# Kernel tuning notes

Measured on AMD Instinct MI355X. Metric: run time of the kernel, lower is better.

The kernel has to match this reference:

```python
import jax, jax.numpy as jnp
import numpy as np

NEG_SLOPE = 0.01
NUM_GRAPHS = 4096


def _gcn(x, W, b, src, dst, ew, n_nodes):
    # GCNConv(normalize=False): linear transform, then weighted scatter-add to targets, plus bias
    h = x @ W                                  # [N, out]
    msg = h[src] * ew[:, None]                 # [E, out] gather + scale
    agg = jax.ops.segment_sum(msg, dst, num_segments=n_nodes)  # scatter-add
    return agg + b


def setup_inputs() -> dict:
    key = jax.random.key(0)
    ks = jax.random.split(key, 24)
    N, E = 253952, 4000000
    x = jax.random.normal(ks[0], (N, 6), dtype=jnp.float32)
    edge_index = jax.random.randint(ks[1], (2, E), 0, N, dtype=jnp.int64)
    edge_weight = jax.random.uniform(ks[2], (E,), dtype=jnp.float32)
    batch = jnp.sort(jax.random.randint(ks[3], (N,), 0, NUM_GRAPHS, dtype=jnp.int64))

    def lin(k, fi, fo):
        k1, k2 = jax.random.split(k)
        s = 1.0 / np.sqrt(fi)
        return (jax.random.normal(k1, (fi, fo), dtype=jnp.float32) * s,
                jax.random.normal(k2, (fo,), dtype=jnp.float32) * s)

    W1, b1 = lin(ks[4], 6, 16)
    W2, b2 = lin(ks[5], 16, 32)
    W3, b3 = lin(ks[6], 32, 64)
    W4, b4 = lin(ks[7], 64, 50)
    Wf1, bf1 = lin(ks[8], 50, 30)
    Wf2, bf2 = lin(ks[9], 30, 20)
    Wf3, bf3 = lin(ks[10], 20, 2)
    return {"x": x, "edge_index": edge_index, "edge_weight": edge_weight, "batch": batch,
            "W1": W1, "b1": b1, "W2": W2, "b2": b2, "W3": W3, "b3": b3, "W4": W4, "b4": b4,
            "Wf1": Wf1, "bf1": bf1, "Wf2": Wf2, "bf2": bf2, "Wf3": Wf3, "bf3": bf3}


def reference(x, edge_index, edge_weight, batch,
              W1, b1, W2, b2, W3, b3, W4, b4,
              Wf1, bf1, Wf2, bf2, Wf3, bf3):
    lrelu = lambda v: jax.nn.leaky_relu(v, NEG_SLOPE)
    src, dst = edge_index[0], edge_index[1]
    n = x.shape[0]
    h = lrelu(_gcn(x, W1, b1, src, dst, edge_weight, n))
    h = lrelu(_gcn(h, W2, b2, src, dst, edge_weight, n))
    h = lrelu(_gcn(h, W3, b3, src, dst, edge_weight, n))
    conv_out = lrelu(_gcn(h, W4, b4, src, dst, edge_weight, n))
    # original applies leaky_relu again (batch_norm is defined but never used)
    h = lrelu(conv_out)
    pooled = jax.ops.segment_sum(h, batch, num_segments=NUM_GRAPHS)  # global_add_pool -> [G, 50]
    out = lrelu(pooled @ Wf1 + bf1)
    # dropout p=0.2 skipped (eval mode)
    out = lrelu(out @ Wf2 + bf2)
    out = lrelu(out @ Wf3 + bf3)
    return out
```

## Files before the change

### kernel.cpp

```cpp
#include <hip/hip_runtime.h>

#define N_NODES 253952
#define N_EDGES 4000000
#define N_GRAPHS 4096
#define NEG_SLOPE 0.01f

#define NB   248
#define CAP  20480
#define EPB  4096
#define WSCALE (1.0f / 16383.0f)

__device__ __forceinline__ float lrelu(float v) {
    return v > 0.0f ? v : v * NEG_SLOPE;
}

__device__ __forceinline__ unsigned short f2bf(float f) {
    unsigned b = __float_as_uint(f);
    return (unsigned short)((b + 0x7FFF + ((b >> 16) & 1)) >> 16);
}

__device__ __forceinline__ float bf2f(unsigned short h) {
    return __uint_as_float((unsigned)h << 16);
}

__device__ __forceinline__ void fma_bf16x8(float acc[8], const uint4 v, const float w) {
    acc[0] += __uint_as_float(v.x << 16) * w;
    acc[1] += __uint_as_float(v.x & 0xFFFF0000u) * w;
    acc[2] += __uint_as_float(v.y << 16) * w;
    acc[3] += __uint_as_float(v.y & 0xFFFF0000u) * w;
    acc[4] += __uint_as_float(v.z << 16) * w;
    acc[5] += __uint_as_float(v.z & 0xFFFF0000u) * w;
    acc[6] += __uint_as_float(v.w << 16) * w;
    acc[7] += __uint_as_float(v.w & 0xFFFF0000u) * w;
}

__global__ void pad_x_kernel(const float* __restrict__ x, unsigned short* __restrict__ xb,
                             int* __restrict__ bucket_cnt) {
    if (blockIdx.x == 0 && threadIdx.x < NB) bucket_cnt[threadIdx.x] = 0;
    int i = blockIdx.x * 256 + threadIdx.x;
    if (i >= N_NODES * 8) return;
    int n = i >> 3, j = i & 7;
    xb[i] = (j < 6) ? f2bf(x[n * 6 + j]) : (unsigned short)0;
}

__global__ void partA_kernel(const int* __restrict__ src, const int* __restrict__ dst,
                             const float* __restrict__ ew,
                             int* __restrict__ bucket_cnt, int2* __restrict__ staging) {
    __shared__ int cnt[NB];
    __shared__ int lds_base[NB + 1];
    __shared__ int gbase[NB];
    __shared__ int cur[NB];
    __shared__ int ss[256];
    __shared__ int2 sorted[EPB];
    const int t = threadIdx.x;
    for (int i = t; i < NB; i += 256) cnt[i] = 0;
    __syncthreads();
    const int e0 = blockIdx.x * EPB;
    int4 s4[4]; int4 d4[4]; float4 w4[4];
#pragma unroll
    for (int k = 0; k < 4; ++k) {
        int e = e0 + 4 * (k * 256 + t);
        if (e + 3 < N_EDGES) {
            s4[k] = *(const int4*)(src + e);
            d4[k] = *(const int4*)(dst + e);
            w4[k] = *(const float4*)(ew + e);
        } else {
            s4[k] = make_int4(0, 0, 0, 0);
            d4[k] = make_int4(-1, -1, -1, -1);
            w4[k] = make_float4(0.f, 0.f, 0.f, 0.f);
            if (e < N_EDGES)     { s4[k].x = src[e];     d4[k].x = dst[e];     w4[k].x = ew[e]; }
            if (e + 1 < N_EDGES) { s4[k].y = src[e + 1]; d4[k].y = dst[e + 1]; w4[k].y = ew[e + 1]; }
            if (e + 2 < N_EDGES) { s4[k].z = src[e + 2]; d4[k].z = dst[e + 2]; w4[k].z = ew[e + 2]; }
        }
    }
#pragma unroll
    for (int k = 0; k < 4; ++k) {
        if (d4[k].x >= 0) atomicAdd(&cnt[d4[k].x >> 10], 1);
        if (d4[k].y >= 0) atomicAdd(&cnt[d4[k].y >> 10], 1);
        if (d4[k].z >= 0) atomicAdd(&cnt[d4[k].z >> 10], 1);
        if (d4[k].w >= 0) atomicAdd(&cnt[d4[k].w >> 10], 1);
    }
    __syncthreads();
    int v = (t < NB) ? cnt[t] : 0;
    ss[t] = v;
    __syncthreads();
    for (int off = 1; off < 256; off <<= 1) {
        int tv = (t >= off) ? ss[t - off] : 0;
        __syncthreads();
        ss[t] += tv;
        __syncthreads();
    }
    if (t < NB) {
        int excl = ss[t] - v;
        lds_base[t] = excl;
        cur[t] = excl;
        gbase[t] = (v > 0) ? atomicAdd(&bucket_cnt[t], v) : 0;
    }
    if (t == 255) lds_base[NB] = ss[255];
    __syncthreads();
#pragma unroll
    for (int k = 0; k < 4; ++k) {
        int d, s; float w;
        d = d4[k].x; s = s4[k].x; w = w4[k].x;
        if (d >= 0) sorted[atomicAdd(&cur[d >> 10], 1)] = make_int2(s | ((d & 1023) << 18), __float_as_int(w));
        d = d4[k].y; s = s4[k].y; w = w4[k].y;
        if (d >= 0) sorted[atomicAdd(&cur[d >> 10], 1)] = make_int2(s | ((d & 1023) << 18), __float_as_int(w));
        d = d4[k].z; s = s4[k].z; w = w4[k].z;
        if (d >= 0) sorted[atomicAdd(&cur[d >> 10], 1)] = make_int2(s | ((d & 1023) << 18), __float_as_int(w));
        d = d4[k].w; s = s4[k].w; w = w4[k].w;
        if (d >= 0) sorted[atomicAdd(&cur[d >> 10], 1)] = make_int2(s | ((d & 1023) << 18), __float_as_int(w));
    }
    __syncthreads();
    const int total = lds_base[NB];
    for (int p = t; p < total; p += 256) {
        int2 r = sorted[p];
        int lo = 0, hi = NB - 1;
        while (lo < hi) { int m = (lo + hi + 1) >> 1; if (lds_base[m] <= p) lo = m; else hi = m - 1; }
        staging[(size_t)lo * CAP + gbase[lo] + (p - lds_base[lo])] = r;
    }
}

__global__ void __launch_bounds__(1024)
partB_kernel(const int2* __restrict__ staging,
             const int* __restrict__ bucket_cnt,
             int* __restrict__ row_start, unsigned* __restrict__ csr) {
    __shared__ int hist[1024];
    __shared__ int ss[256];
    __shared__ int wsum[16];
    __shared__ int s_bbase;
    const int b = blockIdx.x;
    const int t = threadIdx.x;
    int v = 0;
    if (t < 256) { v = (t < NB) ? bucket_cnt[t] : 0; ss[t] = v; }
    __syncthreads();
    for (int off = 1; off < 256; off <<= 1) {
        int tv = (t < 256 && t >= off) ? ss[t - off] : 0;
        __syncthreads();
        if (t < 256) ss[t] += tv;
        __syncthreads();
    }
    if (t == b) s_bbase = ss[t] - v;
    if (b == 0 && t == 0) row_start[N_NODES] = N_EDGES;
    hist[t] = 0;
    __syncthreads();
    const int bbase = s_bbase;
    const int cnt = bucket_cnt[b];
    const int2* rec = staging + (size_t)b * CAP;
    const int4* rec2 = (const int4*)rec;
    const int npair = cnt >> 1;
    for (int i = t; i < npair; i += 1024) {
        int4 pr = rec2[i];
        atomicAdd(&hist[pr.x >> 18], 1);
        atomicAdd(&hist[pr.z >> 18], 1);
    }
    if ((cnt & 1) && t == 0) atomicAdd(&hist[rec[cnt - 1].x >> 18], 1);
    __syncthreads();
    const int lane = t & 63, wid = t >> 6;
    int h = hist[t];
    int val = h;
#pragma unroll
    for (int off = 1; off < 64; off <<= 1) {
        int n = __shfl_up(val, off);
        if (lane >= off) val += n;
    }
    if (lane == 63) wsum[wid] = val;
    __syncthreads();
    if (t < 16) {
        int wv = wsum[t];
#pragma unroll
        for (int off = 1; off < 16; off <<= 1) {
            int n = __shfl_up(wv, off);
            if (t >= off) wv += n;
        }
        wsum[t] = wv;
    }
    __syncthreads();
    int excl = val - h + (wid > 0 ? wsum[wid - 1] : 0);
    row_start[b * 1024 + t] = bbase + excl;
    hist[t] = excl;
    __syncthreads();
    for (int i = t; i < npair; i += 1024) {
        int4 pr = rec2[i];
        int p0 = bbase + atomicAdd(&hist[pr.x >> 18], 1);
        int wq0 = (int)(__int_as_float(pr.y) * 16383.0f + 0.5f);
        wq0 = wq0 < 0 ? 0 : (wq0 > 16383 ? 16383 : wq0);
        csr[p0] = (unsigned)(pr.x & 0x3FFFF) | ((unsigned)wq0 << 18);
        int p1 = bbase + atomicAdd(&hist[pr.z >> 18], 1);
        int wq1 = (int)(__int_as_float(pr.w) * 16383.0f + 0.5f);
        wq1 = wq1 < 0 ? 0 : (wq1 > 16383 ? 16383 : wq1);
        csr[p1] = (unsigned)(pr.z & 0x3FFFF) | ((unsigned)wq1 << 18);
    }
    if ((cnt & 1) && t == 0) {
        int2 r = rec[cnt - 1];
        int pos = bbase + atomicAdd(&hist[r.x >> 18], 1);
        int wq = (int)(__int_as_float(r.y) * 16383.0f + 0.5f);
        wq = wq < 0 ? 0 : (wq > 16383 ? 16383 : wq);
        csr[pos] = (unsigned)(r.x & 0x3FFFF) | ((unsigned)wq << 18);
    }
}

template <int WPAD, int WIN, int WOUT, bool DBL, bool OUT_F32>
__global__ void gcn_layer_kernel(const unsigned short* __restrict__ xb,
                                 const unsigned* __restrict__ csr,
                                 const int* __restrict__ row_start, const int* __restrict__ row_end,
                                 const float* __restrict__ Wg, const float* __restrict__ bg,
                                 void* __restrict__ hout) {
    constexpr int LPN = WPAD / 8;
    constexpr int GROUPS = 256 / LPN;
    __shared__ float rows[GROUPS][WPAD + 4];
    int g = threadIdx.x / LPN;
    int j = threadIdx.x % LPN;
    int node = blockIdx.x * GROUPS + g;
    float acc[8] = {0.f, 0.f, 0.f, 0.f, 0.f, 0.f, 0.f, 0.f};
    int e = row_start[node];
    int end = row_end[node];
    const uint4* xv = (const uint4*)xb;
    for (; e + 4 <= end; e += 4) {
        unsigned r0 = csr[e];
        unsigned r1 = csr[e + 1];
        unsigned r2 = csr[e + 2];
        unsigned r3 = csr[e + 3];
        uint4 v0 = xv[(size_t)(r0 & 0x3FFFFu) * LPN + j];
        uint4 v1 = xv[(size_t)(r1 & 0x3FFFFu) * LPN + j];
        uint4 v2 = xv[(size_t)(r2 & 0x3FFFFu) * LPN + j];
        uint4 v3 = xv[(size_t)(r3 & 0x3FFFFu) * LPN + j];
        fma_bf16x8(acc, v0, (float)(r0 >> 18) * WSCALE);
        fma_bf16x8(acc, v1, (float)(r1 >> 18) * WSCALE);
        fma_bf16x8(acc, v2, (float)(r2 >> 18) * WSCALE);
        fma_bf16x8(acc, v3, (float)(r3 >> 18) * WSCALE);
    }
    for (; e < end; ++e) {
        unsigned r = csr[e];
        uint4 v = xv[(size_t)(r & 0x3FFFFu) * LPN + j];
        fma_bf16x8(acc, v, (float)(r >> 18) * WSCALE);
    }
#pragma unroll
    for (int i = 0; i < 8; ++i) rows[g][8 * j + i] = acc[i];
    __syncthreads();
    for (int idx = threadIdx.x; idx < GROUPS * WOUT; idx += 256) {
        int g2 = idx / WOUT;
        int j2 = idx - g2 * WOUT;
        int node2 = blockIdx.x * GROUPS + g2;
        float a = bg[j2];
#pragma unroll
        for (int k = 0; k < WIN; ++k) a += rows[g2][k] * Wg[k * WOUT + j2];
        a = lrelu(a);
        if (DBL) a = lrelu(a);
        if (OUT_F32) ((float*)hout)[(size_t)node2 * WOUT + j2] = a;
        else ((unsigned short*)hout)[(size_t)node2 * WOUT + j2] = f2bf(a);
    }
}

__global__ void pool_kernel(const unsigned short* __restrict__ h,
                            const int* __restrict__ batch,
                            float* __restrict__ pooled) {
    int g = blockIdx.x;
    __shared__ int s_start, s_end;
    if (threadIdx.x == 0) {
        int lo = 0, hi = N_NODES;
        while (lo < hi) { int m = (lo + hi) >> 1; if (batch[m] < g) lo = m + 1; else hi = m; }
        s_start = lo;
        lo = 0; hi = N_NODES;
        while (lo < hi) { int m = (lo + hi) >> 1; if (batch[m] < g + 1) lo = m + 1; else hi = m; }
        s_end = lo;
    }
    __syncthreads();
    int j = threadIdx.x;
    if (j < 50) {
        float acc = 0.0f;
        for (int i = s_start; i < s_end; ++i) acc += bf2f(h[(size_t)i * 50 + j]);
        pooled[g * 50 + j] = acc;
    }
}

__global__ void mlp_kernel(const float* __restrict__ pooled,
                           const float* __restrict__ Wf1, const float* __restrict__ bf1,
                           const float* __restrict__ Wf2, const float* __restrict__ bf2,
                           const float* __restrict__ Wf3, const float* __restrict__ bf3,
                           float* __restrict__ out) {
    __shared__ float W1s[50 * 30], b1s[30];
    __shared__ float W2s[30 * 20], b2s[20];
    __shared__ float W3s[20 * 2], b3s[2];
    for (int i = threadIdx.x; i < 50 * 30; i += blockDim.x) W1s[i] = Wf1[i];
    for (int i = threadIdx.x; i < 30; i += blockDim.x) b1s[i] = bf1[i];
    for (int i = threadIdx.x; i < 30 * 20; i += blockDim.x) W2s[i] = Wf2[i];
    for (int i = threadIdx.x; i < 20; i += blockDim.x) b2s[i] = bf2[i];
    for (int i = threadIdx.x; i < 20 * 2; i += blockDim.x) W3s[i] = Wf3[i];
    for (int i = threadIdx.x; i < 2; i += blockDim.x) b3s[i] = bf3[i];
    __syncthreads();
    int g = blockIdx.x * blockDim.x + threadIdx.x;
    if (g >= N_GRAPHS) return;
    float in[50];
#pragma unroll
    for (int k = 0; k < 50; ++k) in[k] = pooled[g * 50 + k];
    float t1[30];
#pragma unroll
    for (int j = 0; j < 30; ++j) {
        float a = b1s[j];
#pragma unroll
        for (int k = 0; k < 50; ++k) a += in[k] * W1s[k * 30 + j];
        t1[j] = lrelu(a);
    }
    float t2[20];
#pragma unroll
    for (int j = 0; j < 20; ++j) {
        float a = b2s[j];
#pragma unroll
        for (int k = 0; k < 30; ++k) a += t1[k] * W2s[k * 20 + j];
        t2[j] = lrelu(a);
    }
#pragma unroll
    for (int j = 0; j < 2; ++j) {
        float a = b3s[j];
#pragma unroll
        for (int k = 0; k < 20; ++k) a += t2[k] * W3s[k * 2 + j];
        out[g * 2 + j] = lrelu(a);
    }
}

extern "C" void kernel_launch(void* const* d_in, const int* in_sizes, int n_in,
                              void* d_out, int out_size, void* d_ws, size_t ws_size,
                              hipStream_t stream) {
    const float* x     = (const float*)d_in[0];
    const int*   ei    = (const int*)d_in[1];
    const float* ew    = (const float*)d_in[2];
    const int*   batch = (const int*)d_in[3];
    const float* W1 = (const float*)d_in[4];
    const float* b1 = (const float*)d_in[5];
    const float* W2 = (const float*)d_in[6];
    const float* b2 = (const float*)d_in[7];
    const float* W3 = (const float*)d_in[8];
    const float* b3 = (const float*)d_in[9];
    const float* W4 = (const float*)d_in[10];
    const float* b4 = (const float*)d_in[11];
    const float* Wf1 = (const float*)d_in[12];
    const float* bf1 = (const float*)d_in[13];
    const float* Wf2 = (const float*)d_in[14];
    const float* bf2 = (const float*)d_in[15];
    const float* Wf3 = (const float*)d_in[16];
    const float* bf3 = (const float*)d_in[17];

    const int* src = ei;
    const int* dst = ei + N_EDGES;
    float* out = (float*)d_out;

    char* wsp = (char*)d_ws;
    unsigned* csr     = (unsigned*)wsp;  wsp += (size_t)N_EDGES * 4;
    char*  bufA       = wsp;             wsp += (size_t)N_NODES * 64 * 4;
    char*  bufB       = wsp;             wsp += (size_t)N_NODES * 50 * 4;
    int*   row_start  = (int*)wsp;       wsp += (size_t)(N_NODES + 1) * 4;
    int*   bucket_cnt = (int*)wsp;       wsp += NB * 4;
    float* pooled     = (float*)wsp;

    int2*           staging = (int2*)bufA;
    unsigned short* xb      = (unsigned short*)bufB;
    unsigned short* h1      = (unsigned short*)bufA;
    unsigned short* h2      = (unsigned short*)(bufB + (size_t)N_NODES * 8 * 2);
    unsigned short* h3      = (unsigned short*)bufA;
    unsigned short* h4      = (unsigned short*)bufB;

    const int BS = 256;
    const int ABLK = (N_EDGES + EPB - 1) / EPB;

    pad_x_kernel<<<(N_NODES * 8 + 255) / 256, BS, 0, stream>>>(x, xb, bucket_cnt);
    partA_kernel<<<ABLK, BS, 0, stream>>>(src, dst, ew, bucket_cnt, staging);
    partB_kernel<<<NB, 1024, 0, stream>>>(staging, bucket_cnt, row_start, csr);

    gcn_layer_kernel<8, 6, 16, false, false><<<N_NODES / 256, BS, 0, stream>>>(
        xb, csr, row_start, row_start + 1, W1, b1, h1);
    gcn_layer_kernel<16, 16, 32, false, false><<<N_NODES / 128, BS, 0, stream>>>(
        h1, csr, row_start, row_start + 1, W2, b2, h2);
    gcn_layer_kernel<32, 32, 64, false, false><<<N_NODES / 64, BS, 0, stream>>>(
        h2, csr, row_start, row_start + 1, W3, b3, h3);
    gcn_layer_kernel<64, 64, 50, true, false><<<N_NODES / 32, BS, 0, stream>>>(
        h3, csr, row_start, row_start + 1, W4, b4, h4);

    pool_kernel<<<N_GRAPHS, 64, 0, stream>>>(h4, batch, pooled);
    mlp_kernel<<<(N_GRAPHS + 255) / 256, 256, 0, stream>>>(pooled, Wf1, bf1, Wf2, bf2, Wf3, bf3, out);
}
```

Before: 685.7 us.

## Enlarge partA edge chunk, store bucket ids in LDS, fuse pool with MLP

The edge-bucketing kernel now handles 8192 edges per block, keeping packed records and bucket ids in registers. It also records each sorted entry's bucket in a byte array in LDS, so the per-element binary search during scatter is gone. Global pooling and the three-layer MLP are merged into one kernel per graph, which drops a launch and the round trip of the pooled buffer through global memory. In exchange, partA uses more registers and LDS (64KB+ sorted) and has half as many blocks, which may lower occupancy.

Result: faster. 565.4 us (-17.5%).

```diff
diff --git a/kernel.cpp b/kernel.cpp
--- a/kernel.cpp
+++ b/kernel.cpp
@@ -7,7 +7,7 @@
 
 #define NB   248
 #define CAP  20480
-#define EPB  4096
+#define EPB  8192
 #define WSCALE (1.0f / 16383.0f)
 
 __device__ __forceinline__ float lrelu(float v) {
@@ -43,42 +43,57 @@
     xb[i] = (j < 6) ? f2bf(x[n * 6 + j]) : (unsigned short)0;
 }
 
-__global__ void partA_kernel(const int* __restrict__ src, const int* __restrict__ dst,
-                             const float* __restrict__ ew,
-                             int* __restrict__ bucket_cnt, int2* __restrict__ staging) {
+__global__ void __launch_bounds__(256)
+partA_kernel(const int* __restrict__ src, const int* __restrict__ dst,
+             const float* __restrict__ ew,
+             int* __restrict__ bucket_cnt, int2* __restrict__ staging) {
     __shared__ int cnt[NB];
     __shared__ int lds_base[NB + 1];
     __shared__ int gbase[NB];
     __shared__ int cur[NB];
     __shared__ int ss[256];
     __shared__ int2 sorted[EPB];
+    __shared__ unsigned char sortedb[EPB];
     const int t = threadIdx.x;
     for (int i = t; i < NB; i += 256) cnt[i] = 0;
     __syncthreads();
     const int e0 = blockIdx.x * EPB;
-    int4 s4[4]; int4 d4[4]; float4 w4[4];
-#pragma unroll
-    for (int k = 0; k < 4; ++k) {
+    int2 rec[32];
+    unsigned bkt4[8];
+#pragma unroll
+    for (int k = 0; k < 8; ++k) {
         int e = e0 + 4 * (k * 256 + t);
+        int4 s4; int4 d4; float4 w4;
         if (e + 3 < N_EDGES) {
-            s4[k] = *(const int4*)(src + e);
-            d4[k] = *(const int4*)(dst + e);
-            w4[k] = *(const float4*)(ew + e);
+            s4 = *(const int4*)(src + e);
+            d4 = *(const int4*)(dst + e);
+            w4 = *(const float4*)(ew + e);
         } else {
-            s4[k] = make_int4(0, 0, 0, 0);
-            d4[k] = make_int4(-1, -1, -1, -1);
-            w4[k] = make_float4(0.f, 0.f, 0.f, 0.f);
-            if (e < N_EDGES)     { s4[k].x = src[e];     d4[k].x = dst[e];     w4[k].x = ew[e]; }
-            if (e + 1 < N_EDGES) { s4[k].y = src[e + 1]; d4[k].y = dst[e + 1]; w4[k].y = ew[e + 1]; }
-            if (e + 2 < N_EDGES) { s4[k].z = src[e + 2]; d4[k].z = dst[e + 2]; w4[k].z = ew[e + 2]; }
+            s4 = make_int4(0, 0, 0, 0);
+            d4 = make_int4(-1, -1, -1, -1);
+            w4 = make_float4(0.f, 0.f, 0.f, 0.f);
+            if (e < N_EDGES)     { s4.x = src[e];     d4.x = dst[e];     w4.x = ew[e]; }
+            if (e + 1 < N_EDGES) { s4.y = src[e + 1]; d4.y = dst[e + 1]; w4.y = ew[e + 1]; }
+            if (e + 2 < N_EDGES) { s4.z = src[e + 2]; d4.z = dst[e + 2]; w4.z = ew[e + 2]; }
         }
-    }
-#pragma unroll
-    for (int k = 0; k < 4; ++k) {
-        if (d4[k].x >= 0) atomicAdd(&cnt[d4[k].x >> 10], 1);
-        if (d4[k].y >= 0) atomicAdd(&cnt[d4[k].y >> 10], 1);
-        if (d4[k].z >= 0) atomicAdd(&cnt[d4[k].z >> 10], 1);
-        if (d4[k].w >= 0) atomicAdd(&cnt[d4[k].w >> 10], 1);
+        unsigned b0 = (d4.x >= 0) ? (unsigned)(d4.x >> 10) : 255u;
+        unsigned b1 = (d4.y >= 0) ? (unsigned)(d4.y >> 10) : 255u;
+        unsigned b2 = (d4.z >= 0) ? (unsigned)(d4.z >> 10) : 255u;
+        unsigned b3 = (d4.w >= 0) ? (unsigned)(d4.w >> 10) : 255u;
+        bkt4[k] = b0 | (b1 << 8) | (b2 << 16) | (b3 << 24);
+        rec[4 * k + 0] = make_int2(s4.x | ((d4.x & 1023) << 18), __float_as_int(w4.x));
+        rec[4 * k + 1] = make_int2(s4.y | ((d4.y & 1023) << 18), __float_as_int(w4.y));
+        rec[4 * k + 2] = make_int2(s4.z | ((d4.z & 1023) << 18), __float_as_int(w4.z));
+        rec[4 * k + 3] = make_int2(s4.w | ((d4.w & 1023) << 18), __float_as_int(w4.w));
+    }
+#pragma unroll
+    for (int k = 0; k < 8; ++k) {
+        unsigned bb = bkt4[k];
+        unsigned c0 = bb & 255u, c1 = (bb >> 8) & 255u, c2 = (bb >> 16) & 255u, c3 = bb >> 24;
+        if (c0 != 255u) atomicAdd(&cnt[c0], 1);
+        if (c1 != 255u) atomicAdd(&cnt[c1], 1);
+        if (c2 != 255u) atomicAdd(&cnt[c2], 1);
+        if (c3 != 255u) atomicAdd(&cnt[c3], 1);
     }
     __syncthreads();
     int v = (t < NB) ? cnt[t] : 0;
@@ -99,24 +114,23 @@
     if (t == 255) lds_base[NB] = ss[255];
     __syncthreads();
 #pragma unroll
-    for (int k = 0; k < 4; ++k) {
-        int d, s; float w;
-        d = d4[k].x; s = s4[k].x; w = w4[k].x;
-        if (d >= 0) sorted[atomicAdd(&cur[d >> 10], 1)] = make_int2(s | ((d & 1023) << 18), __float_as_int(w));
-        d = d4[k].y; s = s4[k].y; w = w4[k].y;
-        if (d >= 0) sorted[atomicAdd(&cur[d >> 10], 1)] = make_int2(s | ((d & 1023) << 18), __float_as_int(w));
-        d = d4[k].z; s = s4[k].z; w = w4[k].z;
-        if (d >= 0) sorted[atomicAdd(&cur[d >> 10], 1)] = make_int2(s | ((d & 1023) << 18), __float_as_int(w));
-        d = d4[k].w; s = s4[k].w; w = w4[k].w;
-        if (d >= 0) sorted[atomicAdd(&cur[d >> 10], 1)] = make_int2(s | ((d & 1023) << 18), __float_as_int(w));
+    for (int k = 0; k < 8; ++k) {
+        unsigned bb = bkt4[k];
+#pragma unroll
+        for (int q = 0; q < 4; ++q) {
+            unsigned b = (bb >> (8 * q)) & 255u;
+            if (b != 255u) {
+                int pos = atomicAdd(&cur[b], 1);
+                sorted[pos] = rec[4 * k + q];
+                sortedb[pos] = (unsigned char)b;
+            }
+        }
     }
     __syncthreads();
     const int total = lds_base[NB];
     for (int p = t; p < total; p += 256) {
-        int2 r = sorted[p];
-        int lo = 0, hi = NB - 1;
-        while (lo < hi) { int m = (lo + hi + 1) >> 1; if (lds_base[m] <= p) lo = m; else hi = m - 1; }
-        staging[(size_t)lo * CAP + gbase[lo] + (p - lds_base[lo])] = r;
+        int b = sortedb[p];
+        staging[(size_t)b * CAP + gbase[b] + (p - lds_base[b])] = sorted[p];
     }
 }
 
@@ -251,69 +265,49 @@
     }
 }
 
-__global__ void pool_kernel(const unsigned short* __restrict__ h,
-                            const int* __restrict__ batch,
-                            float* __restrict__ pooled) {
+__global__ void pool_mlp_kernel(const unsigned short* __restrict__ h,
+                                const int* __restrict__ batch,
+                                const float* __restrict__ Wf1, const float* __restrict__ bf1,
+                                const float* __restrict__ Wf2, const float* __restrict__ bf2,
+                                const float* __restrict__ Wf3, const float* __restrict__ bf3,
+                                float* __restrict__ out) {
     int g = blockIdx.x;
-    __shared__ int s_start, s_end;
-    if (threadIdx.x == 0) {
+    __shared__ int bounds[2];
+    __shared__ float pl[50];
+    __shared__ float t1[30];
+    __shared__ float t2[20];
+    int j = threadIdx.x;
+    if (j < 2) {
+        int target = g + j;
         int lo = 0, hi = N_NODES;
-        while (lo < hi) { int m = (lo + hi) >> 1; if (batch[m] < g) lo = m + 1; else hi = m; }
-        s_start = lo;
-        lo = 0; hi = N_NODES;
-        while (lo < hi) { int m = (lo + hi) >> 1; if (batch[m] < g + 1) lo = m + 1; else hi = m; }
-        s_end = lo;
-    }
-    __syncthreads();
-    int j = threadIdx.x;
+        while (lo < hi) { int m = (lo + hi) >> 1; if (batch[m] < target) lo = m + 1; else hi = m; }
+        bounds[j] = lo;
+    }
+    __syncthreads();
     if (j < 50) {
         float acc = 0.0f;
-        for (int i = s_start; i < s_end; ++i) acc += bf2f(h[(size_t)i * 50 + j]);
-        pooled[g * 50 + j] = acc;
-    }
-}
-
-__global__ void mlp_kernel(const float* __restrict__ pooled,
-                           const float* __restrict__ Wf1, const float* __restrict__ bf1,
-                           const float* __restrict__ Wf2, const float* __restrict__ bf2,
-                           const float* __restrict__ Wf3, const float* __restrict__ bf3,
-                           float* __restrict__ out) {
-    __shared__ float W1s[50 * 30], b1s[30];
-    __shared__ float W2s[30 * 20], b2s[20];
-    __shared__ float W3s[20 * 2], b3s[2];
-    for (int i = threadIdx.x; i < 50 * 30; i += blockDim.x) W1s[i] = Wf1[i];
-    for (int i = threadIdx.x; i < 30; i += blockDim.x) b1s[i] = bf1[i];
-    for (int i = threadIdx.x; i < 30 * 20; i += blockDim.x) W2s[i] = Wf2[i];
-    for (int i = threadIdx.x; i < 20; i += blockDim.x) b2s[i] = bf2[i];
-    for (int i = threadIdx.x; i < 20 * 2; i += blockDim.x) W3s[i] = Wf3[i];
-    for (int i = threadIdx.x; i < 2; i += blockDim.x) b3s[i] = bf3[i];
-    __syncthreads();
-    int g = blockIdx.x * blockDim.x + threadIdx.x;
-    if (g >= N_GRAPHS) return;
-    float in[50];
-#pragma unroll
-    for (int k = 0; k < 50; ++k) in[k] = pooled[g * 50 + k];
-    float t1[30];
-#pragma unroll
-    for (int j = 0; j < 30; ++j) {
-        float a = b1s[j];
-#pragma unroll
-        for (int k = 0; k < 50; ++k) a += in[k] * W1s[k * 30 + j];
+        for (int i = bounds[0]; i < bounds[1]; ++i) acc += bf2f(h[(size_t)i * 50 + j]);
+        pl[j] = acc;
+    }
+    __syncthreads();
+    if (j < 30) {
+        float a = bf1[j];
+#pragma unroll
+        for (int k = 0; k < 50; ++k) a += pl[k] * Wf1[k * 30 + j];
         t1[j] = lrelu(a);
     }
-    float t2[20];
-#pragma unroll
-    for (int j = 0; j < 20; ++j) {
-        float a = b2s[j];
-#pragma unroll
-        for (int k = 0; k < 30; ++k) a += t1[k] * W2s[k * 20 + j];
+    __syncthreads();
+    if (j < 20) {
+        float a = bf2[j];
+#pragma unroll
+        for (int k = 0; k < 30; ++k) a += t1[k] * Wf2[k * 20 + j];
         t2[j] = lrelu(a);
     }
-#pragma unroll
-    for (int j = 0; j < 2; ++j) {
-        float a = b3s[j];
-#pragma unroll
-        for (int k = 0; k < 20; ++k) a += t2[k] * W3s[k * 2 + j];
+    __syncthreads();
+    if (j < 2) {
+        float a = bf3[j];
+#pragma unroll
+        for (int k = 0; k < 20; ++k) a += t2[k] * Wf3[k * 2 + j];
         out[g * 2 + j] = lrelu(a);
     }
 }
@@ -350,7 +344,6 @@
     char*  bufB       = wsp;             wsp += (size_t)N_NODES * 50 * 4;
     int*   row_start  = (int*)wsp;       wsp += (size_t)(N_NODES + 1) * 4;
     int*   bucket_cnt = (int*)wsp;       wsp += NB * 4;
-    float* pooled     = (float*)wsp;
 
     int2*           staging = (int2*)bufA;
     unsigned short* xb      = (unsigned short*)bufB;
@@ -375,6 +368,5 @@
     gcn_layer_kernel<64, 64, 50, true, false><<<N_NODES / 32, BS, 0, stream>>>(
         h3, csr, row_start, row_start + 1, W4, b4, h4);
 
-    pool_kernel<<<N_GRAPHS, 64, 0, stream>>>(h4, batch, pooled);
-    mlp_kernel<<<(N_GRAPHS + 255) / 256, 256, 0, stream>>>(pooled, Wf1, bf1, Wf2, bf2, Wf3, bf3, out);
-}
+    pool_mlp_kernel<<<N_GRAPHS, 64, 0, stream>>>(h4, batch, Wf1, bf1, Wf2, bf2, Wf3, bf3, out);
+}
```
